# Performance work log

Measured on AMD Instinct MI355X. Metric: run time of the kernel, lower is better.

## Reference

```python
import jax, jax.numpy as jnp
import numpy as np


def setup_inputs() -> dict:
    N, E, F, M, D = 50000, 200000, 64, 64, 128
    L = 3
    LAMBS = jnp.array([1.0, 0.1, 0.01], jnp.float32) * 12.0  # lambs * output
    R = int(np.ceil(np.sqrt(N)))  # n_virtuals = 224
    RAW = M * L + F  # raw_message_dimension = 256
    key = jax.random.key(0)
    ks = jax.random.split(key, 16)

    def lin(k, i, o):
        return jax.random.normal(k, (i, o), jnp.float32) / np.float32(np.sqrt(i))

    return dict(
        source_nodes=jax.random.randint(ks[0], (E,), 0, N),
        target_nodes=jax.random.randint(ks[1], (E,), 0, N),
        timestamps=jax.random.uniform(ks[2], (E,), jnp.float32),
        now_time=jnp.ones((1,), jnp.float32),
        predict_IND=0,
        node_features=0.1 * jax.random.normal(ks[3], (N, F), jnp.float32),
        memory=jnp.concatenate([0.05 * jax.random.normal(ks[4], (N, L, M), jnp.float32), jnp.ones((N, L, 1), jnp.float32)], axis=-1),
        last_update=jnp.zeros((N,), jnp.float32),
        virtual_memory=0.05 * jax.random.normal(ks[5], (R, L, M), jnp.float32),
        virtual_last_update=jnp.zeros((R,), jnp.float32),
        A_r=jnp.ones((N, R), jnp.float32) + jax.random.uniform(ks[6], (N, R), jnp.float32) / 10.0,
        static_emb=0.1 * jax.random.normal(ks[7], (N, D), jnp.float32),
        lamb=jnp.array([0.5], jnp.float32),
        lambs=LAMBS,
        mf_W1=lin(ks[8], RAW, RAW // 2), mf_b1=jnp.zeros((RAW // 2,), jnp.float32),
        mf_W2=lin(ks[9], RAW // 2, M), mf_b2=jnp.zeros((M,), jnp.float32),
        ffr_W1=lin(ks[10], RAW, RAW), ffr_b1=jnp.zeros((RAW,), jnp.float32),
        ffr_W2=lin(ks[11], RAW, M), ffr_b2=jnp.zeros((M,), jnp.float32),
        et_W=lin(ks[12], L * M, M), et_b=jnp.zeros((M,), jnp.float32),
        st_W=lin(ks[13], 2 * M, D), st_b=jnp.zeros((D,), jnp.float32),
    )


def reference(source_nodes, target_nodes, timestamps, now_time, predict_IND,
              node_features, memory, last_update, virtual_memory, virtual_last_update,
              A_r, static_emb, lamb, lambs,
              mf_W1, mf_b1, mf_W2, mf_b2, ffr_W1, ffr_b1, ffr_W2, ffr_b2,
              et_W, et_b, st_W, st_b):
    N, L, Mp1 = memory.shape
    M = Mp1 - 1
    R = virtual_memory.shape[0]
    E = source_nodes.shape[0]
    eps = 1e-6

    # exp_lambs embedding of targets: memory ratio [E, L*M]
    mem_t = memory[target_nodes]
    tgt_emb = (mem_t[:, :, :-1] / mem_t[:, :, -1:]).reshape(E, L * M)
    # raw message = [target_embedding, node_features[target], 1]  -> [E, RAW+1]
    src_msg = jnp.concatenate([tgt_emb, node_features[target_nodes], jnp.ones((E, 1), tgt_emb.dtype)], axis=1)

    # exp_lambs aggregation: decay every event to the latest timestamp of its source node
    t_max = jax.ops.segment_max(timestamps, source_nodes, num_segments=N)
    cnt = jax.ops.segment_sum(jnp.ones((E,), timestamps.dtype), source_nodes, num_segments=N)
    has_msg = cnt > 0
    t_max = jnp.where(has_msg, t_max, 0.0)
    w = jnp.exp(-lambs[None, :] * (t_max[source_nodes][:, None] - timestamps[:, None]))  # [E, L]
    agg = jax.ops.segment_sum(w[:, :, None] * src_msg[:, None, :], source_nodes, num_segments=N)  # [N, L, RAW+1]

    # MLP message function on feature channels, carry the weight-count channel along
    feat = agg[:, :, :-1]  # [N, L, RAW]
    h = jax.nn.relu(feat @ mf_W1 + mf_b1)
    msg_feat = jax.nn.relu(h @ mf_W2 + mf_b2)  # [N, L, M]
    messages = jnp.concatenate([msg_feat, agg[:, :, -1:]], axis=-1)  # [N, L, M+1]

    # virtual-node routing: A = softmax(A_r, axis=0) restricted to active nodes
    A = jax.nn.softmax(A_r, axis=0) * has_msg[:, None].astype(A_r.dtype)  # [N, R]
    B = jnp.where(has_msg[:, None, None], feat / jnp.maximum(agg[:, :, -1:], eps), 0.0)  # [N, L, RAW]
    vmid = jnp.einsum('nr,nlf->rlf', A, B)  # [R, L, RAW]
    vh = jax.nn.leaky_relu(vmid @ ffr_W1 + ffr_b1)
    vmsg = jax.nn.leaky_relu(vh @ ffr_W2 + ffr_b2)  # [R, L, M]

    # node memory exp-decay update (only active nodes)
    dt = jnp.where(has_msg, t_max - last_update, 0.0)
    decay = jnp.exp(-lambs[None, :, None] * dt[:, None, None])  # [N, L, 1]
    new_mem = jnp.where(has_msg[:, None, None], memory * decay + messages, memory)
    node_emb = (new_mem[:, :, :-1] / jnp.maximum(new_mem[:, :, -1:], eps)).reshape(N, L * M)

    # virtual memory exp-decay update to now_time
    vdt = now_time[0] - virtual_last_update  # [R]
    vdecay = jnp.exp(-lambs[None, :] * vdt[:, None])  # [R, L]
    new_vmem = virtual_memory * vdecay[:, :, None] + vmsg
    v_emb = new_vmem.reshape(R, L * M)

    r2n = jax.nn.softmax(A_r, axis=1)  # [N, R]
    vnode_emb = r2n @ v_emb  # [N, L*M]

    dyn = jnp.concatenate([node_emb, vnode_emb], axis=0)  # [2N, L*M]
    hh = jax.nn.leaky_relu(dyn @ et_W + et_b)  # [2N, M]
    hh = hh.reshape(2, N, M).transpose(1, 0, 2).reshape(N, 2 * M)
    spat = jax.nn.leaky_relu(hh @ st_W + st_b)  # [N, D]
    return lamb[0] * static_emb + (1.0 - lamb[0]) * spat
```

## Files before the change

### kernel.cpp

```cpp
#include <hip/hip_runtime.h>

static __device__ __forceinline__ float lky(float x) { return x > 0.f ? x : 0.01f * x; }

static __device__ __forceinline__ unsigned short f2bf(float x) {
    unsigned int u = __float_as_uint(x);
    unsigned int r = (u + 0x7FFFu + ((u >> 16) & 1u)) >> 16;
    return (unsigned short)r;
}
static __device__ __forceinline__ float bf2f(unsigned short x) {
    return __uint_as_float((unsigned int)x << 16);
}
static __device__ __forceinline__ unsigned int pack2bf(float lo, float hi) {
    return (unsigned int)f2bf(lo) | ((unsigned int)f2bf(hi) << 16);
}

typedef __attribute__((ext_vector_type(8))) short short8;
typedef __attribute__((ext_vector_type(4))) float f32x4;

constexpr int SN  = 50048;
constexpr int KLV = 608;
constexpr int VCM = 83;
constexpr int NSCAN = 53248;
constexpr int NWG_V = 12 * VCM;
constexpr int NQ_V  = NWG_V / 8;
constexpr int NR_V  = NWG_V % 8;

__global__ void k_init(float* t_max, int* cnt, int* cursor, float* colsum, int N, int NP) {
    int i = blockIdx.x * 256 + threadIdx.x;
    if (i < N) { t_max[i] = -1.0f; cursor[i] = 0; }
    if (i < NP) cnt[i] = 0;
    if (i < 224) colsum[i] = 0.0f;
}

__global__ void k_tbf(const float* __restrict__ src, unsigned short* __restrict__ dst,
                      int K, int C) {
    int i = blockIdx.x * 256 + threadIdx.x;
    if (i >= K * C) return;
    int c = i / K, k = i % K;
    dst[i] = f2bf(src[k * C + c]);
}

__global__ void k_tmax_cnt(const int* __restrict__ src, const float* __restrict__ ts,
                           float* t_max, int* cnt, int E) {
    int e = blockIdx.x * 256 + threadIdx.x;
    if (e >= E) return;
    int s = src[e];
    atomicMax((int*)(t_max + s), __float_as_int(ts[e]));
    atomicAdd(cnt + s, 1);
}

__global__ __launch_bounds__(1024) void k_scan(const int* __restrict__ cnt,
                                               int* __restrict__ offsets, int N) {
    __shared__ int wsum[16];
    __shared__ int s_run;
    int t = threadIdx.x;
    int lane = t & 63, wid = t >> 6;
    if (t == 0) s_run = 0;
    __syncthreads();
    int nchunk = (N + 4095) >> 12;
    for (int c = 0; c < nchunk; ++c) {
        int i0 = (c << 12) + t * 4;
        int4 v = *(const int4*)(cnt + i0);
        int s = v.x + v.y + v.z + v.w;
        int x = s;
        #pragma unroll
        for (int d = 1; d < 64; d <<= 1) {
            int y = __shfl_up(x, d, 64);
            if (lane >= d) x += y;
        }
        if (lane == 63) wsum[wid] = x;
        __syncthreads();
        int wbase = 0;
        #pragma unroll
        for (int w = 0; w < 16; ++w) wbase += (w < wid) ? wsum[w] : 0;
        int run = s_run;
        int base = run + wbase + x - s;
        if (i0 + 3 < N) {
            int4 o;
            o.x = base; o.y = base + v.x; o.z = o.y + v.y; o.w = o.z + v.z;
            *(int4*)(offsets + i0) = o;
        } else {
            int o = base;
            if (i0 < N) offsets[i0] = o;
            o += v.x;
            if (i0 + 1 < N) offsets[i0 + 1] = o;
            o += v.y;
            if (i0 + 2 < N) offsets[i0 + 2] = o;
            o += v.z;
            if (i0 + 3 < N) offsets[i0 + 3] = o;
        }
        __syncthreads();
        if (t == 1023) s_run = run + wbase + x;
        __syncthreads();
    }
    if (t == 0) offsets[N] = s_run;
}

__global__ void k_scatter(const int* __restrict__ src, const int* __restrict__ offsets,
                          int* cursor, int* sorted, int E) {
    int e = blockIdx.x * 256 + threadIdx.x;
    if (e >= E) return;
    int s = src[e];
    int pos = offsets[s] + atomicAdd(cursor + s, 1);
    sorted[pos] = e;
}

__global__ __launch_bounds__(256) void k_prep(
        const float* __restrict__ memory, const float* __restrict__ nodef,
        unsigned int* __restrict__ temb, int N) {
    int wid = threadIdx.x >> 6, lane = threadIdx.x & 63;
    int n = blockIdx.x * 4 + wid;
    if (n >= N) return;
    const float* mrow = memory + (size_t)n * 195;
    float d0 = mrow[64], d1 = mrow[129], d2 = mrow[194];
    int f = 2 * lane;
    float den = (f < 64) ? d0 : d1;
    int offA = (f < 64) ? f : f + 1;
    float va0 = mrow[offA] / den;
    float va1 = mrow[offA + 1] / den;
    float vb0, vb1;
    if (lane < 32) {
        vb0 = mrow[130 + 2 * lane] / d2;
        vb1 = mrow[131 + 2 * lane] / d2;
    } else {
        const float* nf = nodef + (size_t)n * 64 + 2 * (lane - 32);
        vb0 = nf[0]; vb1 = nf[1];
    }
    temb[(size_t)n * 128 + lane]      = pack2bf(va0, va1);
    temb[(size_t)n * 128 + 64 + lane] = pack2bf(vb0, vb1);
}

__global__ __launch_bounds__(256) void k_aexp(
        const float* __restrict__ A_r,
        float* __restrict__ rowsum, float* __restrict__ colsum,
        unsigned short* __restrict__ AexpT, unsigned short* __restrict__ Aexp_rm, int N) {
    __shared__ unsigned short sE[64][228];
    int t = threadIdx.x;
    int n0 = blockIdx.x * 64;
    int maxq = min(64, N - n0) * 56;
    const float4* src = (const float4*)(A_r + (size_t)n0 * 224);
    #pragma unroll
    for (int k = 0; k < 14; ++k) {
        int i = t + k * 256;
        float4 v = (i < maxq) ? src[i] : (float4){-1e30f, -1e30f, -1e30f, -1e30f};
        int row = i / 56, cq = i % 56;
        uint2 pk;
        pk.x = pack2bf(__expf(v.x), __expf(v.y));
        pk.y = pack2bf(__expf(v.z), __expf(v.w));
        *(uint2*)&sE[row][cq * 4] = pk;
    }
    __syncthreads();
    {
        int row = t >> 2, q = t & 3;
        const uint2* p = (const uint2*)&sE[row][q * 56];
        float s = 0.f;
        #pragma unroll
        for (int c = 0; c < 7; ++c) {
            uint2 u = p[c];
            s += __uint_as_float(u.x << 16) + __uint_as_float(u.x & 0xffff0000u)
               + __uint_as_float(u.y << 16) + __uint_as_float(u.y & 0xffff0000u);
        }
        s += __shfl_xor(s, 1, 64);
        s += __shfl_xor(s, 2, 64);
        if (q == 0 && n0 + row < N) rowsum[n0 + row] = s;
    }
    if (t < 224) {
        float s = 0.f;
        #pragma unroll 8
        for (int r = 0; r < 64; ++r) s += bf2f(sE[r][t]);
        atomicAdd(colsum + t, s);
    }
    {
        unsigned int* dst = (unsigned int*)Aexp_rm;
        for (int i = t; i < 64 * 112; i += 256) {
            int n = i / 112, cp = i % 112;
            dst[(size_t)(n0 + n) * 112 + cp] = *(const unsigned int*)&sE[n][2 * cp];
        }
    }
    {
        unsigned int* dst = (unsigned int*)AexpT;
        for (int u = t; u < 224 * 32; u += 256) {
            int r = u >> 5, np = u & 31;
            unsigned int lo = sE[2 * np][r];
            unsigned int hi = sE[2 * np + 1][r];
            dst[(size_t)r * (SN / 2) + (n0 >> 1) + np] = lo | (hi << 16);
        }
    }
}

__global__ __launch_bounds__(256) void k_agg(
        const int* __restrict__ tgt, const float* __restrict__ ts,
        const int* __restrict__ sorted, const int* __restrict__ offsets,
        const float* __restrict__ t_max, const unsigned int* __restrict__ temb,
        const float* __restrict__ lambs,
        unsigned int* __restrict__ aggb, float* __restrict__ cnt3,
        int* __restrict__ has_msg, int N) {
    int wid = threadIdx.x >> 6, lane = threadIdx.x & 63;
    int n = blockIdx.x * 4 + wid;
    size_t rb = (size_t)n * 3;
    if (n >= N) {
        #pragma unroll
        for (int l = 0; l < 3; ++l) {
            unsigned int* row = aggb + (rb + l) * 128;
            row[lane] = 0; row[64 + lane] = 0;
            if (lane == 0) cnt3[rb + l] = 0.f;
        }
        return;
    }
    int beg = offsets[n], end = offsets[n + 1];
    float lb0 = lambs[0], lb1 = lambs[1], lb2 = lambs[2];
    float tm = t_max[n];
    float aa0[3], aa1[3], ab0[3], ab1[3], accc[3];
    #pragma unroll
    for (int l = 0; l < 3; ++l) { aa0[l] = aa1[l] = ab0[l] = ab1[l] = accc[l] = 0.f; }
    for (int idx = beg; idx < end; ++idx) {
        int e = sorted[idx];
        int tt = tgt[e];
        float d = tm - ts[e];
        unsigned int ua = temb[(size_t)tt * 128 + lane];
        unsigned int ub = temb[(size_t)tt * 128 + 64 + lane];
        float a0 = __uint_as_float(ua << 16);
        float a1 = __uint_as_float(ua & 0xffff0000u);
        float b0 = __uint_as_float(ub << 16);
        float b1 = __uint_as_float(ub & 0xffff0000u);
        float w0 = __expf(-lb0 * d), w1 = __expf(-lb1 * d), w2 = __expf(-lb2 * d);
        aa0[0] += w0 * a0; aa1[0] += w0 * a1; ab0[0] += w0 * b0; ab1[0] += w0 * b1; accc[0] += w0;
        aa0[1] += w1 * a0; aa1[1] += w1 * a1; ab0[1] += w1 * b0; ab1[1] += w1 * b1; accc[1] += w1;
        aa0[2] += w2 * a0; aa1[2] += w2 * a1; ab0[2] += w2 * b0; ab1[2] += w2 * b1; accc[2] += w2;
    }
    #pragma unroll
    for (int l = 0; l < 3; ++l) {
        unsigned int* row = aggb + (rb + l) * 128;
        row[lane]      = pack2bf(aa0[l], aa1[l]);
        row[64 + lane] = pack2bf(ab0[l], ab1[l]);
        if (lane == 0) cnt3[rb + l] = accc[l];
    }
    if (lane == 0) has_msg[n] = (end > beg) ? 1 : 0;
}

__global__ __launch_bounds__(256) void k_mf_mfma(
        const unsigned short* __restrict__ aggb,
        const unsigned short* __restrict__ W1T, const float* __restrict__ b1,
        const unsigned short* __restrict__ W2T, const float* __restrict__ b2,
        unsigned short* __restrict__ msg_feat, int NROWS) {
    __shared__ unsigned short As[32 * 264];
    __shared__ unsigned short Hs[32 * 136];
    int t = threadIdx.x, lane = t & 63, w = t >> 6;
    int lr = lane & 15, kg = lane >> 4;
    int row0 = blockIdx.x * 32;
    {
        int r = t >> 3, s8 = t & 7;
        const uint4* src = (const uint4*)(aggb + (size_t)(row0 + r) * 256 + s8 * 32);
        uint4* dst = (uint4*)(As + r * 264 + s8 * 32);
        #pragma unroll
        for (int u = 0; u < 4; ++u) dst[u] = src[u];
    }
    __syncthreads();
    int n0 = w * 32;
    f32x4 acc[2][2];
    #pragma unroll
    for (int m = 0; m < 2; ++m) {
        acc[m][0] = (f32x4){0.f, 0.f, 0.f, 0.f};
        acc[m][1] = (f32x4){0.f, 0.f, 0.f, 0.f};
    }
    for (int kk = 0; kk < 8; ++kk) {
        short8 bf0 = *(const short8*)(W1T + (size_t)(n0 + lr) * 256 + kk * 32 + kg * 8);
        short8 bf1 = *(const short8*)(W1T + (size_t)(n0 + 16 + lr) * 256 + kk * 32 + kg * 8);
        #pragma unroll
        for (int m = 0; m < 2; ++m) {
            short8 af = *(const short8*)(As + (m * 16 + lr) * 264 + kk * 32 + kg * 8);
            acc[m][0] = __builtin_amdgcn_mfma_f32_16x16x32_bf16(af, bf0, acc[m][0], 0, 0, 0);
            acc[m][1] = __builtin_amdgcn_mfma_f32_16x16x32_bf16(af, bf1, acc[m][1], 0, 0, 0);
        }
    }
    float bb0 = b1[n0 + lr], bb1 = b1[n0 + 16 + lr];
    #pragma unroll
    for (int m = 0; m < 2; ++m)
        #pragma unroll
        for (int j = 0; j < 4; ++j) {
            int row = m * 16 + kg * 4 + j;
            Hs[row * 136 + n0 + lr]      = f2bf(fmaxf(acc[m][0][j] + bb0, 0.f));
            Hs[row * 136 + n0 + 16 + lr] = f2bf(fmaxf(acc[m][1][j] + bb1, 0.f));
        }
    __syncthreads();
    int c0 = w * 16;
    f32x4 a2[2];
    #pragma unroll
    for (int m = 0; m < 2; ++m) a2[m] = (f32x4){0.f, 0.f, 0.f, 0.f};
    for (int kk = 0; kk < 4; ++kk) {
        short8 bf = *(const short8*)(W2T + (size_t)(c0 + lr) * 128 + kk * 32 + kg * 8);
        #pragma unroll
        for (int m = 0; m < 2; ++m) {
            short8 af = *(const short8*)(Hs + (m * 16 + lr) * 136 + kk * 32 + kg * 8);
            a2[m] = __builtin_amdgcn_mfma_f32_16x16x32_bf16(af, bf, a2[m], 0, 0, 0);
        }
    }
    float b2v = b2[c0 + lr];
    #pragma unroll
    for (int m = 0; m < 2; ++m)
        #pragma unroll
        for (int j = 0; j < 4; ++j) {
            int row = row0 + m * 16 + kg * 4 + j;
            if (row < NROWS)
                msg_feat[(size_t)row * 64 + c0 + lr] = f2bf(fmaxf(a2[m][j] + b2v, 0.f));
        }
}

__global__ __launch_bounds__(256) void k_vmid_mfma(
        const unsigned short* __restrict__ AexpT, const unsigned short* __restrict__ aggb,
        const float* __restrict__ cnt3, float* __restrict__ vpart) {
    __shared__ unsigned short As[112 * 40];
    __shared__ unsigned int BsT[128 * 20];
    int bx = blockIdx.x;
    int xcd = bx & 7, bidx = bx >> 3;
    int virt = (xcd < NR_V) ? xcd * (NQ_V + 1) + bidx
                            : NR_V * (NQ_V + 1) + (xcd - NR_V) * NQ_V + bidx;
    int chunk = virt / 12, tile = virt % 12;
    int r0 = (tile & 1) * 112;
    int ft = tile >> 1;
    int l = ft >> 1, fo = (ft & 1) * 128;
    int t = threadIdx.x, lane = t & 63, w = t >> 6;
    int lr = lane & 15, kg = lane >> 4;
    int np = t >> 4, sg = t & 15;
    f32x4 acc[7][2];
    #pragma unroll
    for (int q = 0; q < 7; ++q) {
        acc[q][0] = (f32x4){0.f, 0.f, 0.f, 0.f};
        acc[q][1] = (f32x4){0.f, 0.f, 0.f, 0.f};
    }
    int nbeg = chunk * KLV;
    int nsteps = min(KLV, SN - nbeg) >> 5;
    int c0 = w * 32 + lr, c1 = c0 + 16;
    int rb0 = c0 * 20 + (kg ^ ((c0 >> 3) & 3)) * 4;
    int rb1 = c1 * 20 + (kg ^ ((c1 >> 3) & 3)) * 4;
    int swz = np ^ ((sg & 3) << 2);
    for (int s = 0; s < nsteps; ++s) {
        int n0 = nbeg + s * 32;
        if (t < 224) {
            int srow = t >> 1, sseg = t & 1;
            const uint4* ap = (const uint4*)(AexpT + (size_t)(r0 + srow) * SN + n0) + sseg * 2;
            uint4 v0 = ap[0];
            uint4 v1 = ap[1];
            *(uint4*)&As[srow * 40 + sseg * 16]     = v0;
            *(uint4*)&As[srow * 40 + sseg * 16 + 8] = v1;
        }
        {
            int na = n0 + 2 * np;
            size_t ra = ((size_t)na * 3 + l) * 256 + fo + sg * 8;
            uint4 va = *(const uint4*)(aggb + ra);
            uint4 vb = *(const uint4*)(aggb + ra + 768);
            float da = 1.f / fmaxf(cnt3[(size_t)na * 3 + l], 1e-6f);
            float db = 1.f / fmaxf(cnt3[(size_t)na * 3 + l + 3], 1e-6f);
            const unsigned short* pa = (const unsigned short*)&va;
            const unsigned short* pb = (const unsigned short*)&vb;
            unsigned int* dst = BsT + sg * 160 + swz;
            #pragma unroll
            for (int j = 0; j < 8; ++j)
                dst[j * 20] = pack2bf(bf2f(pa[j]) * da, bf2f(pb[j]) * db);
        }
        __syncthreads();
        short8 b0 = *(const short8*)((const unsigned short*)(BsT + rb0));
        short8 b1 = *(const short8*)((const unsigned short*)(BsT + rb1));
        #pragma unroll
        for (int q = 0; q < 7; ++q) {
            short8 af = *(const short8*)&As[(q * 16 + lr) * 40 + kg * 8];
            acc[q][0] = __builtin_amdgcn_mfma_f32_16x16x32_bf16(af, b0, acc[q][0], 0, 0, 0);
            acc[q][1] = __builtin_amdgcn_mfma_f32_16x16x32_bf16(af, b1, acc[q][1], 0, 0, 0);
        }
        __syncthreads();
    }
    float* outp = vpart + (size_t)chunk * 172032;
    #pragma unroll
    for (int q = 0; q < 7; ++q) {
        int row = r0 + q * 16 + kg * 4;
        #pragma unroll
        for (int p = 0; p < 2; ++p) {
            int col = l * 256 + fo + w * 32 + p * 16 + lr;
            #pragma unroll
            for (int j = 0; j < 4; ++j)
                outp[(size_t)(row + j) * 768 + col] = acc[q][p][j];
        }
    }
}

__global__ void k_vred(const float* __restrict__ vpart, const float* __restrict__ colsum,
                       float* __restrict__ vmid) {
    int idx = blockIdx.x * 256 + threadIdx.x;
    if (idx >= 224 * 768) return;
    float s = 0.f;
    for (int c = 0; c < VCM; ++c) s += vpart[(long)c * (224 * 768) + idx];
    vmid[idx] = s / colsum[idx / 768];
}

__global__ __launch_bounds__(256) void k_ffr(
        const float* __restrict__ vmid, const float* __restrict__ W1, const float* __restrict__ b1,
        const float* __restrict__ W2, const float* __restrict__ b2,
        const float* __restrict__ vmem, const float* __restrict__ vlast,
        const float* __restrict__ lambs, const float* __restrict__ now_time,
        unsigned short* __restrict__ vembT) {
    __shared__ float sin_[16][260];
    __shared__ float svh[16][260];
    int row0 = blockIdx.x * 16;
    int t = threadIdx.x;
    #pragma unroll
    for (int k = 0; k < 16; ++k) {
        int idx = t + k * 256;
        int r = idx >> 8, f = idx & 255;
        sin_[r][f] = vmid[(long)(row0 + r) * 256 + f];
    }
    __syncthreads();
    {
        int cg = t & 63, rg = t >> 6;
        int c0 = cg * 4, r0 = rg * 4;
        float acc[4][4];
        #pragma unroll
        for (int i = 0; i < 4; ++i)
            #pragma unroll
            for (int j = 0; j < 4; ++j) acc[i][j] = 0.f;
        for (int f0 = 0; f0 < 256; f0 += 4) {
            float4 a[4];
            #pragma unroll
            for (int i = 0; i < 4; ++i) a[i] = *(const float4*)&sin_[r0 + i][f0];
            #pragma unroll
            for (int ff = 0; ff < 4; ++ff) {
                float4 w = *(const float4*)&W1[(long)(f0 + ff) * 256 + c0];
                #pragma unroll
                for (int i = 0; i < 4; ++i) {
                    float av = (&a[i].x)[ff];
                    acc[i][0] += av * w.x; acc[i][1] += av * w.y;
                    acc[i][2] += av * w.z; acc[i][3] += av * w.w;
                }
            }
        }
        #pragma unroll
        for (int i = 0; i < 4; ++i)
            #pragma unroll
            for (int j = 0; j < 4; ++j)
                svh[r0 + i][c0 + j] = lky(acc[i][j] + b1[c0 + j]);
    }
    __syncthreads();
    {
        int cg = t & 31, rg = t >> 5;
        int c0 = cg * 2, r0 = rg * 2;
        float acc[2][2];
        acc[0][0] = acc[0][1] = acc[1][0] = acc[1][1] = 0.f;
        for (int f0 = 0; f0 < 256; f0 += 4) {
            float4 a[2];
            #pragma unroll
            for (int i = 0; i < 2; ++i) a[i] = *(const float4*)&svh[r0 + i][f0];
            #pragma unroll
            for (int ff = 0; ff < 4; ++ff) {
                float2 w = *(const float2*)&W2[(long)(f0 + ff) * 64 + c0];
                #pragma unroll
                for (int i = 0; i < 2; ++i) {
                    float av = (&a[i].x)[ff];
                    acc[i][0] += av * w.x; acc[i][1] += av * w.y;
                }
            }
        }
        float nowv = now_time[0];
        #pragma unroll
        for (int i = 0; i < 2; ++i) {
            int row = row0 + r0 + i;
            int rr = row / 3, l = row % 3;
            float vd = __expf(-lambs[l] * (nowv - vlast[rr]));
            #pragma unroll
            for (int j = 0; j < 2; ++j) {
                float v = lky(acc[i][j] + b2[c0 + j]);
                int m = c0 + j;
                vembT[(size_t)(l * 64 + m) * 224 + rr] =
                    f2bf(vmem[(long)rr * 192 + l * 64 + m] * vd + v);
            }
        }
    }
}

__global__ void k_newmem(const float* __restrict__ memory,
        const unsigned short* __restrict__ msg_feat,
        const float* __restrict__ cnt3, const float* __restrict__ t_max,
        const float* __restrict__ last_update, const int* __restrict__ has_msg,
        const float* __restrict__ lambs, unsigned short* __restrict__ node_emb, int N) {
    int n = blockIdx.x;
    int j = threadIdx.x;
    int l = j >> 6, m = j & 63;
    int has = has_msg[n];
    float dt = has ? (t_max[n] - last_update[n]) : 0.f;
    float decay = __expf(-lambs[l] * dt);
    long mb = (long)n * 195 + l * 65;
    float num = memory[mb + m];
    float den = memory[mb + 64];
    if (has) {
        num = num * decay + bf2f(msg_feat[(size_t)n * 192 + j]);
        den = den * decay + cnt3[(size_t)n * 3 + l];
    }
    node_emb[(size_t)n * 192 + j] = f2bf(num / fmaxf(den, 1e-6f));
}

__global__ __launch_bounds__(256) void k_vnode_mfma(
        const unsigned short* __restrict__ Aexp_rm, const unsigned short* __restrict__ vembT,
        const float* __restrict__ rowsum, unsigned short* __restrict__ vnode_emb, int N) {
    __shared__ unsigned short As[64 * 232];
    __shared__ float sRS[64];
    int t = threadIdx.x, lane = t & 63, w = t >> 6;
    int lr = lane & 15, kg = lane >> 4;
    int row0 = blockIdx.x * 64;
    {
        int r = t >> 2, sg = t & 3;
        const uint4* src = (const uint4*)(Aexp_rm + (size_t)(row0 + r) * 224 + sg * 56);
        uint4* dst = (uint4*)(As + r * 232 + sg * 56);
        #pragma unroll
        for (int u = 0; u < 7; ++u) dst[u] = src[u];
    }
    if (t < 64) sRS[t] = rowsum[min(row0 + t, N - 1)];
    __syncthreads();
    int n0 = w * 48;
    f32x4 acc[4][3];
    #pragma unroll
    for (int m = 0; m < 4; ++m)
        #pragma unroll
        for (int nt = 0; nt < 3; ++nt) acc[m][nt] = (f32x4){0.f, 0.f, 0.f, 0.f};
    for (int kk = 0; kk < 7; ++kk) {
        short8 bf[3];
        #pragma unroll
        for (int nt = 0; nt < 3; ++nt)
            bf[nt] = *(const short8*)(vembT + (size_t)(n0 + nt * 16 + lr) * 224 + kk * 32 + kg * 8);
        #pragma unroll
        for (int m = 0; m < 4; ++m) {
            short8 af = *(const short8*)(As + (m * 16 + lr) * 232 + kk * 32 + kg * 8);
            #pragma unroll
            for (int nt = 0; nt < 3; ++nt)
                acc[m][nt] = __builtin_amdgcn_mfma_f32_16x16x32_bf16(af, bf[nt], acc[m][nt], 0, 0, 0);
        }
    }
    #pragma unroll
    for (int m = 0; m < 4; ++m)
        #pragma unroll
        for (int j = 0; j < 4; ++j) {
            int row = row0 + m * 16 + kg * 4 + j;
            if (row < N) {
                float inv = 1.f / sRS[row - row0];
                #pragma unroll
                for (int nt = 0; nt < 3; ++nt)
                    vnode_emb[(size_t)row * 192 + n0 + nt * 16 + lr] = f2bf(acc[m][nt][j] * inv);
            }
        }
}

__global__ __launch_bounds__(256) void k_et_st_mfma(
        const unsigned short* __restrict__ ne, const unsigned short* __restrict__ ve,
        const unsigned short* __restrict__ etWT, const float* __restrict__ etb,
        const unsigned short* __restrict__ stWT, const float* __restrict__ stb,
        const float* __restrict__ stat, const float* __restrict__ lamb,
        float* __restrict__ out, int N) {
    __shared__ unsigned short As[64 * 200];
    __shared__ unsigned short Hs[32 * 136];
    int t = threadIdx.x, lane = t & 63, w = t >> 6;
    int lr = lane & 15, kg = lane >> 4;
    int row0 = blockIdx.x * 32;
    {
        int r = t >> 3, s8 = t & 7;
        const uint4* sn = (const uint4*)(ne + (size_t)(row0 + r) * 192 + s8 * 24);
        const uint4* sv = (const uint4*)(ve + (size_t)(row0 + r) * 192 + s8 * 24);
        uint4* dn = (uint4*)(As + (size_t)r * 200 + s8 * 24);
        uint4* dv = (uint4*)(As + (size_t)(32 + r) * 200 + s8 * 24);
        #pragma unroll
        for (int u = 0; u < 3; ++u) { dn[u] = sn[u]; dv[u] = sv[u]; }
    }
    __syncthreads();
    int c0 = w * 16;
    f32x4 acc[2][2];
    #pragma unroll
    for (int h = 0; h < 2; ++h)
        #pragma unroll
        for (int m = 0; m < 2; ++m) acc[h][m] = (f32x4){0.f, 0.f, 0.f, 0.f};
    for (int kk = 0; kk < 6; ++kk) {
        short8 bf = *(const short8*)(etWT + (size_t)(c0 + lr) * 192 + kk * 32 + kg * 8);
        #pragma unroll
        for (int h = 0; h < 2; ++h)
            #pragma unroll
            for (int m = 0; m < 2; ++m) {
                short8 af = *(const short8*)(As + (size_t)(h * 32 + m * 16 + lr) * 200 + kk * 32 + kg * 8);
                acc[h][m] = __builtin_amdgcn_mfma_f32_16x16x32_bf16(af, bf, acc[h][m], 0, 0, 0);
            }
    }
    float bb = etb[c0 + lr];
    #pragma unroll
    for (int h = 0; h < 2; ++h)
        #pragma unroll
        for (int m = 0; m < 2; ++m)
            #pragma unroll
            for (int j = 0; j < 4; ++j)
                Hs[(m * 16 + kg * 4 + j) * 136 + h * 64 + c0 + lr] = f2bf(lky(acc[h][m][j] + bb));
    __syncthreads();
    int c0s = w * 32;
    f32x4 a2[2][2];
    #pragma unroll
    for (int m = 0; m < 2; ++m) { a2[m][0] = (f32x4){0.f,0.f,0.f,0.f}; a2[m][1] = (f32x4){0.f,0.f,0.f,0.f}; }
    for (int kk = 0; kk < 4; ++kk) {
        short8 bf0 = *(const short8*)(stWT + (size_t)(c0s + lr) * 128 + kk * 32 + kg * 8);
        short8 bf1 = *(const short8*)(stWT + (size_t)(c0s + 16 + lr) * 128 + kk * 32 + kg * 8);
        #pragma unroll
        for (int m = 0; m < 2; ++m) {
            short8 af = *(const short8*)(Hs + (m * 16 + lr) * 136 + kk * 32 + kg * 8);
            a2[m][0] = __builtin_amdgcn_mfma_f32_16x16x32_bf16(af, bf0, a2[m][0], 0, 0, 0);
            a2[m][1] = __builtin_amdgcn_mfma_f32_16x16x32_bf16(af, bf1, a2[m][1], 0, 0, 0);
        }
    }
    float lam = lamb[0];
    float sb0 = stb[c0s + lr], sb1 = stb[c0s + 16 + lr];
    #pragma unroll
    for (int m = 0; m < 2; ++m)
        #pragma unroll
        for (int j = 0; j < 4; ++j) {
            int n = row0 + m * 16 + kg * 4 + j;
            if (n < N) {
                int ca = c0s + lr, cb = c0s + 16 + lr;
                float va = lky(a2[m][0][j] + sb0);
                float vb = lky(a2[m][1][j] + sb1);
                out[(size_t)n * 128 + ca] = lam * stat[(size_t)n * 128 + ca] + (1.f - lam) * va;
                out[(size_t)n * 128 + cb] = lam * stat[(size_t)n * 128 + cb] + (1.f - lam) * vb;
            }
        }
}

extern "C" void kernel_launch(void* const* d_in, const int* in_sizes, int n_in,
                              void* d_out, int out_size, void* d_ws, size_t ws_size,
                              hipStream_t stream) {
    const int*   src        = (const int*)d_in[0];
    const int*   tgt        = (const int*)d_in[1];
    const float* ts         = (const float*)d_in[2];
    const float* now_time   = (const float*)d_in[3];
    const float* nodef      = (const float*)d_in[5];
    const float* memory     = (const float*)d_in[6];
    const float* last_upd   = (const float*)d_in[7];
    const float* vmem       = (const float*)d_in[8];
    const float* vlast      = (const float*)d_in[9];
    const float* A_r        = (const float*)d_in[10];
    const float* static_emb = (const float*)d_in[11];
    const float* lamb       = (const float*)d_in[12];
    const float* lambs      = (const float*)d_in[13];
    const float* mf_W1      = (const float*)d_in[14];
    const float* mf_b1      = (const float*)d_in[15];
    const float* mf_W2      = (const float*)d_in[16];
    const float* mf_b2      = (const float*)d_in[17];
    const float* ffr_W1     = (const float*)d_in[18];
    const float* ffr_b1     = (const float*)d_in[19];
    const float* ffr_W2     = (const float*)d_in[20];
    const float* ffr_b2     = (const float*)d_in[21];
    const float* et_W       = (const float*)d_in[22];
    const float* et_b       = (const float*)d_in[23];
    const float* st_W       = (const float*)d_in[24];
    const float* st_b       = (const float*)d_in[25];

    int E = in_sizes[0];
    int N = in_sizes[7];

    float* ws = (float*)d_ws;
    size_t off = 0;
    auto alloc = [&](size_t nf) { float* p = ws + off; off += (nf + 63) & ~(size_t)63; return p; };
    unsigned short* aggb  = (unsigned short*)alloc((size_t)SN * 384);
    unsigned short* msg_feat = (unsigned short*)alloc((size_t)N * 96);
    unsigned short* AexpT   = (unsigned short*)alloc((size_t)224 * SN / 2);
    unsigned short* Aexp_rm = (unsigned short*)alloc((size_t)SN * 224 / 2);
    float* tv_union = alloc((size_t)VCM * 172032);
    float* vmid     = alloc(224 * 768);
    unsigned short* vembT = (unsigned short*)alloc((size_t)192 * 224 / 2 + 64);
    float* t_max    = alloc(N);
    float* rowsum   = alloc(N);
    float* cnt3     = alloc((size_t)SN * 3);
    float* colsum   = alloc(256);
    unsigned short* W1T  = (unsigned short*)alloc(128 * 256 / 2);
    unsigned short* W2T  = (unsigned short*)alloc(64 * 128 / 2);
    unsigned short* etWT = (unsigned short*)alloc(64 * 192 / 2);
    unsigned short* stWT = (unsigned short*)alloc(128 * 128 / 2);
    int*   cnt      = (int*)alloc(NSCAN);
    int*   offsets  = (int*)alloc(N + 1);
    int*   cursor   = (int*)alloc(N);
    int*   sorted   = (int*)alloc(E);
    int*   has_msg  = (int*)alloc(N);
    if (off * sizeof(float) > ws_size) return;

    unsigned int* temb = (unsigned int*)tv_union;
    float* vpart = tv_union;
    unsigned short* node_emb  = (unsigned short*)aggb;
    unsigned short* vnode_emb = node_emb + (size_t)N * 192;

    k_init<<<(NSCAN + 255) / 256, 256, 0, stream>>>(t_max, cnt, cursor, colsum, N, NSCAN);
    k_tbf<<<(256 * 128 + 255) / 256, 256, 0, stream>>>(mf_W1, W1T, 256, 128);
    k_tbf<<<(128 * 64 + 255) / 256, 256, 0, stream>>>(mf_W2, W2T, 128, 64);
    k_tbf<<<(192 * 64 + 255) / 256, 256, 0, stream>>>(et_W, etWT, 192, 64);
    k_tbf<<<(128 * 128 + 255) / 256, 256, 0, stream>>>(st_W, stWT, 128, 128);
    k_tmax_cnt<<<(E + 255) / 256, 256, 0, stream>>>(src, ts, t_max, cnt, E);
    k_scan<<<1, 1024, 0, stream>>>(cnt, offsets, N);
    k_scatter<<<(E + 255) / 256, 256, 0, stream>>>(src, offsets, cursor, sorted, E);
    k_prep<<<(N + 3) / 4, 256, 0, stream>>>(memory, nodef, temb, N);
    k_aexp<<<SN / 64, 256, 0, stream>>>(A_r, rowsum, colsum, AexpT, Aexp_rm, N);
    k_agg<<<SN / 4, 256, 0, stream>>>(tgt, ts, sorted, offsets, t_max, temb,
                                      lambs, (unsigned int*)aggb, cnt3, has_msg, N);
    k_mf_mfma<<<SN * 3 / 32, 256, 0, stream>>>(aggb, W1T, mf_b1, W2T, mf_b2, msg_feat, N * 3);
    k_vmid_mfma<<<NWG_V, 256, 0, stream>>>(AexpT, aggb, cnt3, vpart);
    k_vred<<<(224 * 768 + 255) / 256, 256, 0, stream>>>(vpart, colsum, vmid);
    k_ffr<<<42, 256, 0, stream>>>(vmid, ffr_W1, ffr_b1, ffr_W2, ffr_b2, vmem, vlast,
                                  lambs, now_time, vembT);
    k_newmem<<<N, 192, 0, stream>>>(memory, msg_feat, cnt3, t_max, last_upd, has_msg,
                                    lambs, node_emb, N);
    k_vnode_mfma<<<SN / 64, 256, 0, stream>>>(Aexp_rm, vembT, rowsum, vnode_emb, N);
    k_et_st_mfma<<<SN / 32, 256, 0, stream>>>(node_emb, vnode_emb, etWT, et_b, stWT, st_b,
                                              static_emb, lamb, (float*)d_out, N);
}
```

Baseline: 381.8 us.

## Process 128 rows per block in message MLP with register-resident weights and prefetch

Each block of the message-function MLP kernel now handles 128 rows as two 64-row tiles instead of 32 rows. The W1/W2 bf16 fragments are loaded into registers once per block rather than reloaded from global memory in every k-step. The second tile's input rows are prefetched into registers while the first tile computes. The aim is to cut redundant weight traffic and hide global load latency, at the cost of much higher register use and fewer blocks, which may lower occupancy.

```diff
diff --git a/kernel.cpp b/kernel.cpp
--- a/kernel.cpp
+++ b/kernel.cpp
@@ -243,67 +243,90 @@
         const unsigned short* __restrict__ W1T, const float* __restrict__ b1,
         const unsigned short* __restrict__ W2T, const float* __restrict__ b2,
         unsigned short* __restrict__ msg_feat, int NROWS) {
-    __shared__ unsigned short As[32 * 264];
-    __shared__ unsigned short Hs[32 * 136];
+    __shared__ unsigned short As[64 * 264];
+    __shared__ unsigned short Hs[64 * 136];
     int t = threadIdx.x, lane = t & 63, w = t >> 6;
     int lr = lane & 15, kg = lane >> 4;
-    int row0 = blockIdx.x * 32;
+    int row0 = blockIdx.x * 128;
+    int n0 = w * 32, c0 = w * 16;
+    short8 bw1[8][2], bw2[4];
+    #pragma unroll
+    for (int kk = 0; kk < 8; ++kk) {
+        bw1[kk][0] = *(const short8*)(W1T + (size_t)(n0 + lr) * 256 + kk * 32 + kg * 8);
+        bw1[kk][1] = *(const short8*)(W1T + (size_t)(n0 + 16 + lr) * 256 + kk * 32 + kg * 8);
+    }
+    #pragma unroll
+    for (int kk = 0; kk < 4; ++kk)
+        bw2[kk] = *(const short8*)(W2T + (size_t)(c0 + lr) * 128 + kk * 32 + kg * 8);
+    int r = t >> 2, s4 = t & 3;
+    uint4* dstA = (uint4*)(As + r * 264 + s4 * 64);
+    uint4 pre[8];
     {
-        int r = t >> 3, s8 = t & 7;
-        const uint4* src = (const uint4*)(aggb + (size_t)(row0 + r) * 256 + s8 * 32);
-        uint4* dst = (uint4*)(As + r * 264 + s8 * 32);
-        #pragma unroll
-        for (int u = 0; u < 4; ++u) dst[u] = src[u];
+        const uint4* g0 = (const uint4*)(aggb + (size_t)(row0 + r) * 256 + s4 * 64);
+        #pragma unroll
+        for (int u = 0; u < 8; ++u) pre[u] = g0[u];
+        #pragma unroll
+        for (int u = 0; u < 8; ++u) dstA[u] = pre[u];
     }
     __syncthreads();
-    int n0 = w * 32;
-    f32x4 acc[2][2];
-    #pragma unroll
-    for (int m = 0; m < 2; ++m) {
-        acc[m][0] = (f32x4){0.f, 0.f, 0.f, 0.f};
-        acc[m][1] = (f32x4){0.f, 0.f, 0.f, 0.f};
-    }
-    for (int kk = 0; kk < 8; ++kk) {
-        short8 bf0 = *(const short8*)(W1T + (size_t)(n0 + lr) * 256 + kk * 32 + kg * 8);
-        short8 bf1 = *(const short8*)(W1T + (size_t)(n0 + 16 + lr) * 256 + kk * 32 + kg * 8);
-        #pragma unroll
-        for (int m = 0; m < 2; ++m) {
-            short8 af = *(const short8*)(As + (m * 16 + lr) * 264 + kk * 32 + kg * 8);
-            acc[m][0] = __builtin_amdgcn_mfma_f32_16x16x32_bf16(af, bf0, acc[m][0], 0, 0, 0);
-            acc[m][1] = __builtin_amdgcn_mfma_f32_16x16x32_bf16(af, bf1, acc[m][1], 0, 0, 0);
-        }
-    }
     float bb0 = b1[n0 + lr], bb1 = b1[n0 + 16 + lr];
-    #pragma unroll
-    for (int m = 0; m < 2; ++m)
-        #pragma unroll
-        for (int j = 0; j < 4; ++j) {
-            int row = m * 16 + kg * 4 + j;
-            Hs[row * 136 + n0 + lr]      = f2bf(fmaxf(acc[m][0][j] + bb0, 0.f));
-            Hs[row * 136 + n0 + 16 + lr] = f2bf(fmaxf(acc[m][1][j] + bb1, 0.f));
-        }
-    __syncthreads();
-    int c0 = w * 16;
-    f32x4 a2[2];
-    #pragma unroll
-    for (int m = 0; m < 2; ++m) a2[m] = (f32x4){0.f, 0.f, 0.f, 0.f};
-    for (int kk = 0; kk < 4; ++kk) {
-        short8 bf = *(const short8*)(W2T + (size_t)(c0 + lr) * 128 + kk * 32 + kg * 8);
-        #pragma unroll
-        for (int m = 0; m < 2; ++m) {
-            short8 af = *(const short8*)(Hs + (m * 16 + lr) * 136 + kk * 32 + kg * 8);
-            a2[m] = __builtin_amdgcn_mfma_f32_16x16x32_bf16(af, bf, a2[m], 0, 0, 0);
-        }
-    }
     float b2v = b2[c0 + lr];
     #pragma unroll
-    for (int m = 0; m < 2; ++m)
-        #pragma unroll
-        for (int j = 0; j < 4; ++j) {
-            int row = row0 + m * 16 + kg * 4 + j;
-            if (row < NROWS)
-                msg_feat[(size_t)row * 64 + c0 + lr] = f2bf(fmaxf(a2[m][j] + b2v, 0.f));
-        }
+    for (int tile = 0; tile < 2; ++tile) {
+        if (tile == 0) {
+            const uint4* g1 = (const uint4*)(aggb + (size_t)(row0 + 64 + r) * 256 + s4 * 64);
+            #pragma unroll
+            for (int u = 0; u < 8; ++u) pre[u] = g1[u];
+        }
+        f32x4 acc[4][2];
+        #pragma unroll
+        for (int m = 0; m < 4; ++m) {
+            acc[m][0] = (f32x4){0.f, 0.f, 0.f, 0.f};
+            acc[m][1] = (f32x4){0.f, 0.f, 0.f, 0.f};
+        }
+        #pragma unroll
+        for (int kk = 0; kk < 8; ++kk)
+            #pragma unroll
+            for (int m = 0; m < 4; ++m) {
+                short8 af = *(const short8*)(As + (m * 16 + lr) * 264 + kk * 32 + kg * 8);
+                acc[m][0] = __builtin_amdgcn_mfma_f32_16x16x32_bf16(af, bw1[kk][0], acc[m][0], 0, 0, 0);
+                acc[m][1] = __builtin_amdgcn_mfma_f32_16x16x32_bf16(af, bw1[kk][1], acc[m][1], 0, 0, 0);
+            }
+        #pragma unroll
+        for (int m = 0; m < 4; ++m)
+            #pragma unroll
+            for (int j = 0; j < 4; ++j) {
+                int row = m * 16 + kg * 4 + j;
+                Hs[row * 136 + n0 + lr]      = f2bf(fmaxf(acc[m][0][j] + bb0, 0.f));
+                Hs[row * 136 + n0 + 16 + lr] = f2bf(fmaxf(acc[m][1][j] + bb1, 0.f));
+            }
+        __syncthreads();
+        f32x4 a2[4];
+        #pragma unroll
+        for (int m = 0; m < 4; ++m) a2[m] = (f32x4){0.f, 0.f, 0.f, 0.f};
+        #pragma unroll
+        for (int kk = 0; kk < 4; ++kk)
+            #pragma unroll
+            for (int m = 0; m < 4; ++m) {
+                short8 af = *(const short8*)(Hs + (m * 16 + lr) * 136 + kk * 32 + kg * 8);
+                a2[m] = __builtin_amdgcn_mfma_f32_16x16x32_bf16(af, bw2[kk], a2[m], 0, 0, 0);
+            }
+        int rbase = row0 + tile * 64;
+        #pragma unroll
+        for (int m = 0; m < 4; ++m)
+            #pragma unroll
+            for (int j = 0; j < 4; ++j) {
+                int row = rbase + m * 16 + kg * 4 + j;
+                if (row < NROWS)
+                    msg_feat[(size_t)row * 64 + c0 + lr] = f2bf(fmaxf(a2[m][j] + b2v, 0.f));
+            }
+        if (tile == 0) {
+            __syncthreads();
+            #pragma unroll
+            for (int u = 0; u < 8; ++u) dstA[u] = pre[u];
+            __syncthreads();
+        }
+    }
 }
 
 __global__ __launch_bounds__(256) void k_vmid_mfma(
@@ -697,7 +720,7 @@
     k_aexp<<<SN / 64, 256, 0, stream>>>(A_r, rowsum, colsum, AexpT, Aexp_rm, N);
     k_agg<<<SN / 4, 256, 0, stream>>>(tgt, ts, sorted, offsets, t_max, temb,
                                       lambs, (unsigned int*)aggb, cnt3, has_msg, N);
-    k_mf_mfma<<<SN * 3 / 32, 256, 0, stream>>>(aggb, W1T, mf_b1, W2T, mf_b2, msg_feat, N * 3);
+    k_mf_mfma<<<SN * 3 / 128, 256, 0, stream>>>(aggb, W1T, mf_b1, W2T, mf_b2, msg_feat, N * 3);
     k_vmid_mfma<<<NWG_V, 256, 0, stream>>>(AexpT, aggb, cnt3, vpart);
     k_vred<<<(224 * 768 + 255) / 256, 256, 0, stream>>>(vpart, colsum, vmid);
     k_ffr<<<42, 256, 0, stream>>>(vmid, ffr_W1, ffr_b1, ffr_W2, ffr_b2, vmem, vlast,
```

After: 389.2 us. No clear change (+1.9%).
